# Optimization experiments

Hardware: AMD Instinct MI355X
Metric: run time of the kernel (lower is better)

The kernel has to match this reference:

```python
import jax, jax.numpy as jnp
import numpy as np

H = 16
QK_NOPE = 128
QK_ROPE = 64
QK_HEAD = 192
V_HEAD = 128
KV_LORA = 512
Q_LORA = 1536
HIDDEN = 2048
ROPE_THETA = 500000.0
EPS = 1e-6


def _rms_norm(x, w, eps=EPS):
    var = jnp.mean(x * x, axis=-1, keepdims=True)
    return w * (x * jax.lax.rsqrt(var + eps))


def _rotate_half(x):
    d = x.shape[-1] // 2
    return jnp.concatenate([-x[..., d:], x[..., :d]], axis=-1)


def _rope_cos_sin(T, dim, theta, dtype):
    inv_freq = 1.0 / (theta ** (jnp.arange(0, dim, 2, dtype=jnp.float32) / dim))
    t = jnp.arange(T, dtype=jnp.float32)
    freqs = jnp.outer(t, inv_freq)               # [T, dim//2]
    emb = jnp.concatenate([freqs, freqs], axis=-1)  # [T, dim]
    return jnp.cos(emb).astype(dtype), jnp.sin(emb).astype(dtype)


def _apply_rope_interleave(q, k, cos, sin):
    # deinterleave: [x0,x1,x2,...] -> [x0,x2,... , x1,x3,...]
    def deint(x):
        return jnp.concatenate([x[..., 0::2], x[..., 1::2]], axis=-1)
    q, k = deint(q), deint(k)
    cos = cos[None, None]  # [1,1,T,d]
    sin = sin[None, None]
    q_e = q * cos + _rotate_half(q) * sin
    k_e = k * cos + _rotate_half(k) * sin
    return q_e, k_e


def setup_inputs() -> dict:
    key = jax.random.key(0)
    ks = jax.random.split(key, 8)
    s = 0.02
    B, T = 2, 2048
    return {
        "x": jax.random.normal(ks[0], (B, T, HIDDEN), jnp.float32),
        "q_a_w": jax.random.normal(ks[1], (HIDDEN, Q_LORA), jnp.float32) * s,
        "q_a_ln_w": jnp.ones((Q_LORA,), jnp.float32),
        "q_b_w": jax.random.normal(ks[2], (Q_LORA, H * QK_HEAD), jnp.float32) * s,
        "kv_a_w": jax.random.normal(ks[3], (HIDDEN, KV_LORA + QK_ROPE), jnp.float32) * s,
        "kv_a_ln_w": jnp.ones((KV_LORA,), jnp.float32),
        "kv_b_w": jax.random.normal(ks[4], (KV_LORA, H * (QK_NOPE + V_HEAD)), jnp.float32) * s,
        "o_w": jax.random.normal(ks[5], (H * V_HEAD, HIDDEN), jnp.float32) * s,
    }


def reference(x, q_a_w, q_a_ln_w, q_b_w, kv_a_w, kv_a_ln_w, kv_b_w, o_w):
    B, T, _ = x.shape
    scale = QK_HEAD ** -0.5

    # Q path: hidden -> q_lora -> RMSNorm -> H*qk_head
    q = _rms_norm(x @ q_a_w, q_a_ln_w) @ q_b_w
    q = q.reshape(B, T, H, QK_HEAD).transpose(0, 2, 1, 3)  # [B,H,T,qk_head]
    q_nope, q_rope = q[..., :QK_NOPE], q[..., QK_NOPE:]

    # KV path: hidden -> kv_lora + rope_dim
    ckv = x @ kv_a_w
    kv_c, k_rope = ckv[..., :KV_LORA], ckv[..., KV_LORA:]
    kv = _rms_norm(kv_c, kv_a_ln_w) @ kv_b_w
    kv = kv.reshape(B, T, H, QK_NOPE + V_HEAD).transpose(0, 2, 1, 3)
    k_nope, v = kv[..., :QK_NOPE], kv[..., QK_NOPE:]

    k_rope = k_rope.reshape(B, 1, T, QK_ROPE)
    cos, sin = _rope_cos_sin(T, QK_ROPE, ROPE_THETA, x.dtype)
    q_rope, k_rope = _apply_rope_interleave(q_rope, k_rope, cos, sin)
    k_rope = jnp.broadcast_to(k_rope, (B, H, T, QK_ROPE))

    qf = jnp.concatenate([q_nope, q_rope], axis=-1)  # [B,H,T,192]
    kf = jnp.concatenate([k_nope, k_rope], axis=-1)

    # causal SDPA
    scores = jnp.einsum("bhqd,bhkd->bhqk", qf, kf) * scale
    causal = jnp.tril(jnp.ones((T, T), bool))
    scores = jnp.where(causal[None, None], scores, jnp.finfo(scores.dtype).min)
    attn = jax.nn.softmax(scores, axis=-1)
    out = jnp.einsum("bhqk,bhkd->bhqd", attn, v)  # [B,H,T,128]
    out = out.transpose(0, 2, 1, 3).reshape(B, T, H * V_HEAD)
    return out @ o_w
```

## Files before the change

kernel.cpp:

```cpp
#include <hip/hip_runtime.h>
#include <hip/hip_bf16.h>
#include <cstdint>


typedef __bf16 bf16;
typedef __bf16 bf16x8 __attribute__((ext_vector_type(8)));
typedef __bf16 bf16x4v __attribute__((ext_vector_type(4)));
typedef float f32x4 __attribute__((ext_vector_type(4)));

#define TSEQ 2048
#define MR 4096

typedef const uint32_t __attribute__((address_space(1))) * gas1_t;
typedef uint32_t __attribute__((address_space(3))) * las3_t;

static __device__ __forceinline__ void gload_lds16(const void* g, void* l) {
  __builtin_amdgcn_global_load_lds(
      reinterpret_cast<gas1_t>(reinterpret_cast<uintptr_t>(g)),
      reinterpret_cast<las3_t>(reinterpret_cast<uintptr_t>(l)), 16, 0, 0);
}

static __device__ __forceinline__ f32x4 mfma16(bf16x8 a, bf16x8 b, f32x4 c) {
  return __builtin_amdgcn_mfma_f32_16x16x32_bf16(a, b, c, 0, 0, 0);
}

static __device__ __forceinline__ void do_transpose(
    const float* __restrict__ W, bf16* __restrict__ Wt, int K, int N, int bi,
    int bj, float (*t)[33]) {
  int c = threadIdx.x & 31, r0 = threadIdx.x >> 5;
#pragma unroll
  for (int rr = 0; rr < 32; rr += 8)
    t[rr + r0][c] = W[(size_t)(bj * 32 + rr + r0) * N + bi * 32 + c];
  __syncthreads();
#pragma unroll
  for (int rr = 0; rr < 32; rr += 8)
    Wt[(size_t)(bi * 32 + rr + r0) * K + bj * 32 + c] = (bf16)t[c][rr + r0];
}

#define PREP_BLOCKS (8192 + 3072 + 1152 + 4608 + 2048 + 4096 + 192 + 256)

__global__ __launch_bounds__(256) void k_prep(
    const float* __restrict__ x, const float* __restrict__ q_a_w,
    const float* __restrict__ kv_a_w, const float* __restrict__ q_b_w,
    const float* __restrict__ kv_b_w, const float* __restrict__ o_w,
    bf16* __restrict__ x_bf, bf16* __restrict__ ab_wt,
    bf16* __restrict__ qb_wt, bf16* __restrict__ kvb_wt,
    bf16* __restrict__ o_wt, float* __restrict__ rt) {
  __shared__ float t[32][33];
  int nb = blockIdx.x;
  const int tid = threadIdx.x;
  if (nb < 8192) {
    int i = nb * 256 + tid;
    float4 f = reinterpret_cast<const float4*>(x)[i];
    bf16x4v o = {(bf16)f.x, (bf16)f.y, (bf16)f.z, (bf16)f.w};
    reinterpret_cast<bf16x4v*>(x_bf)[i] = o;
    return;
  }
  nb -= 8192;
  if (nb < 3072) { do_transpose(q_a_w, ab_wt, 2048, 1536, nb % 48, nb / 48, t); return; }
  nb -= 3072;
  if (nb < 1152) {
    do_transpose(kv_a_w, ab_wt + (size_t)1536 * 2048, 2048, 576, nb % 18, nb / 18, t);
    return;
  }
  nb -= 1152;
  if (nb < 4608) { do_transpose(q_b_w, qb_wt, 1536, 3072, nb % 96, nb / 96, t); return; }
  nb -= 4608;
  if (nb < 2048) { do_transpose(kv_b_w, kvb_wt, 512, 4096, nb % 128, nb / 128, t); return; }
  nb -= 2048;
  if (nb < 4096) { do_transpose(o_w, o_wt, 2048, 2048, nb % 64, nb / 64, t); return; }
  nb -= 4096;
  if (nb < 192) {
    uint4 z = make_uint4(0, 0, 0, 0);
    reinterpret_cast<uint4*>(ab_wt + (size_t)2112 * 2048)[nb * 256 + tid] = z;
    return;
  }
  nb -= 192;
  {
    int idx = nb * 256 + tid;
    int tt = idx >> 5, j = idx & 31;
    float freq = exp2f(-(float)j * (1.0f / 32.0f) * log2f(500000.0f));
    float ang = (float)tt * freq;
    rt[tt * 64 + 2 * j] = cosf(ang);
    rt[tt * 64 + 2 * j + 1] = sinf(ang);
  }
}

template <int NCH>
__global__ __launch_bounds__(64) void k_rmsnorm(const bf16* __restrict__ in,
                                                const float* __restrict__ w,
                                                bf16* __restrict__ out,
                                                int in_stride) {
  int row = blockIdx.x, lane = threadIdx.x;
  const int D = NCH * 512;
  const bf16* ip = in + (size_t)row * in_stride;
  bf16x8 v[NCH];
  float ss = 0.f;
#pragma unroll
  for (int c = 0; c < NCH; ++c) {
    v[c] = *reinterpret_cast<const bf16x8*>(ip + c * 512 + lane * 8);
#pragma unroll
    for (int e = 0; e < 8; ++e) { float f = (float)v[c][e]; ss += f * f; }
  }
#pragma unroll
  for (int m = 1; m <= 32; m <<= 1) ss += __shfl_xor(ss, m);
  float rs = rsqrtf(ss / (float)D + 1e-6f);
  bf16* op = out + (size_t)row * D;
#pragma unroll
  for (int c = 0; c < NCH; ++c) {
    bf16x8 o;
#pragma unroll
    for (int e = 0; e < 8; ++e)
      o[e] = (bf16)((float)v[c][e] * rs * w[c * 512 + lane * 8 + e]);
    *reinterpret_cast<bf16x8*>(op + c * 512 + lane * 8) = o;
  }
}

__global__ __launch_bounds__(64) void k_kv_norm_rope(
    const bf16* __restrict__ in, const float* __restrict__ w,
    const float* __restrict__ rt, bf16* __restrict__ kvn,
    bf16* __restrict__ kr, int in_stride) {
  int row = blockIdx.x, lane = threadIdx.x;
  const bf16* ip = in + (size_t)row * in_stride;
  bf16x8 v = *reinterpret_cast<const bf16x8*>(ip + lane * 8);
  float ss = 0.f;
#pragma unroll
  for (int e = 0; e < 8; ++e) { float f = (float)v[e]; ss += f * f; }
#pragma unroll
  for (int m = 1; m <= 32; m <<= 1) ss += __shfl_xor(ss, m);
  float rs = rsqrtf(ss / 512.0f + 1e-6f);
  bf16x8 o;
#pragma unroll
  for (int e = 0; e < 8; ++e) o[e] = (bf16)((float)v[e] * rs * w[lane * 8 + e]);
  *reinterpret_cast<bf16x8*>(kvn + (size_t)row * 512 + lane * 8) = o;
  if (lane < 32) {
    int t = row & (TSEQ - 1);
    float x0 = (float)ip[512 + 2 * lane], x1 = (float)ip[512 + 2 * lane + 1];
    float c = rt[t * 64 + 2 * lane], s = rt[t * 64 + 2 * lane + 1];
    kr[(size_t)row * 64 + lane] = (bf16)(x0 * c - x1 * s);
    kr[(size_t)row * 64 + 32 + lane] = (bf16)(x1 * c + x0 * s);
  }
}

__global__ __launch_bounds__(256) void k_rope_q(const bf16* __restrict__ q,
                                                const float* __restrict__ rt,
                                                bf16* __restrict__ qr) {
  int idx = blockIdx.x * 256 + threadIdx.x;
  int j = idx & 31, h = (idx >> 5) & 15, row = idx >> 9;
  int t = row & (TSEQ - 1);
  const bf16* src = q + (size_t)row * 3072 + h * 192 + 128;
  float x0 = (float)src[2 * j], x1 = (float)src[2 * j + 1];
  float c = rt[t * 64 + 2 * j], s = rt[t * 64 + 2 * j + 1];
  bf16* dst = qr + ((size_t)row * 16 + h) * 64;
  dst[j] = (bf16)(x0 * c - x1 * s);
  dst[32 + j] = (bf16)(x1 * c + x0 * s);
}

#define GPH(BUF, MH, KH, DO_READB, STAGE_STMT, WAIT_STMT)                     \
  {                                                                           \
    if (DO_READB) {                                                           \
      _Pragma("unroll") for (int ni = 0; ni < 4; ++ni) {                      \
        int row = wn * 64 + ni * 16 + lr;                                     \
        breg[KH][ni] = *reinterpret_cast<const bf16x8*>(                      \
            &Bs[BUF][row * 64 + ((((KH)*4 + lg) ^ (row & 7)) * 8)]);          \
      }                                                                       \
    }                                                                         \
    bf16x8 af[4];                                                             \
    _Pragma("unroll") for (int mi = 0; mi < 4; ++mi) {                        \
      int row = wm * 128 + (MH)*64 + mi * 16 + lr;                            \
      af[mi] = *reinterpret_cast<const bf16x8*>(                              \
          &As[BUF][row * 64 + ((((KH)*4 + lg) ^ (row & 7)) * 8)]);            \
    }                                                                         \
    STAGE_STMT;                                                               \
    __builtin_amdgcn_s_barrier();                                             \
    __builtin_amdgcn_s_setprio(1);                                            \
    _Pragma("unroll") for (int mi = 0; mi < 4; ++mi)                          \
        _Pragma("unroll") for (int ni = 0; ni < 4; ++ni)                      \
            acc[(MH)*4 + mi][ni] =                                            \
        mfma16(af[mi], breg[KH][ni], acc[(MH)*4 + mi][ni]);                   \
    __builtin_amdgcn_s_setprio(0);                                            \
    WAIT_STMT;                                                                \
    __builtin_amdgcn_s_barrier();                                             \
  }

template <bool OUT_F32>
__global__ __launch_bounds__(512, 2) void k_gemm8(const bf16* __restrict__ A,
                                                  const bf16* __restrict__ Bt,
                                                  void* __restrict__ C, int M,
                                                  int N, int K) {
  __shared__ bf16 As[2][256 * 64];
  __shared__ bf16 Bs[2][256 * 64];
  const int tid = threadIdx.x, lane = tid & 63, w = tid >> 6;
  const int lg = lane >> 4, lr = lane & 15;
  const int wm = w >> 2, wn = w & 3;
  const int nwg = gridDim.x * gridDim.y;
  const int orig = blockIdx.y * gridDim.x + blockIdx.x;
  const int cpx = nwg >> 3;
  const int wgid = (orig & 7) * cpx + (orig >> 3);
  const int m0 = (wgid / gridDim.x) * 256, n0 = (wgid % gridDim.x) * 256;
  const int T = K >> 7;

  f32x4 acc[8][4] = {};
  bf16x8 breg[2][4];

  auto stageA = [&](int tau, int h) {
    char* dst = (char*)&As[tau & 1][0] + h * 16384;
#pragma unroll
    for (int j = 0; j < 2; ++j) {
      int c = j * 512 + tid;
      int row = c >> 3, slot = c & 7;
      gload_lds16(A + (size_t)(m0 + h * 128 + row) * K + tau * 64 +
                      ((slot ^ (row & 7)) * 8),
                  dst + (size_t)(j * 512 + w * 64) * 16);
    }
  };
  auto stageB = [&](int tau, int h) {
    char* dst = (char*)&Bs[tau & 1][0] + h * 16384;
#pragma unroll
    for (int j = 0; j < 2; ++j) {
      int c = j * 512 + tid;
      int row = c >> 3, slot = c & 7;
      gload_lds16(Bt + (size_t)(n0 + h * 128 + row) * K + tau * 64 +
                      ((slot ^ (row & 7)) * 8),
                  dst + (size_t)(j * 512 + w * 64) * 16);
    }
  };

  stageB(0, 0); stageB(0, 1); stageA(0, 0); stageA(0, 1);
  stageB(1, 0); stageB(1, 1); stageA(1, 0);
  asm volatile("s_waitcnt vmcnt(6)" ::: "memory");
  __builtin_amdgcn_s_barrier();

  for (int t = 0; t < T - 1; ++t) {
    const int s2 = 2 * t + 2, s3 = 2 * t + 3, a1 = 2 * t + 1;
    GPH(0, 0, 0, true,  stageA(a1, 1), ((void)0));
    GPH(0, 0, 1, true,  stageB(s2, 0), ((void)0));
    GPH(0, 1, 0, false, stageB(s2, 1), ((void)0));
    GPH(0, 1, 1, false, stageA(s2, 0),
        asm volatile("s_waitcnt vmcnt(6)" ::: "memory"));
    GPH(1, 0, 0, true,  stageA(s2, 1), ((void)0));
    GPH(1, 0, 1, true,  stageB(s3, 0), ((void)0));
    GPH(1, 1, 0, false, stageB(s3, 1), ((void)0));
    GPH(1, 1, 1, false, stageA(s3, 0),
        asm volatile("s_waitcnt vmcnt(6)" ::: "memory"));
  }
  {
    const int a1 = 2 * T - 1;
    GPH(0, 0, 0, true,  stageA(a1, 1), ((void)0));
    GPH(0, 0, 1, true,  ((void)0),     ((void)0));
    GPH(0, 1, 0, false, ((void)0),     ((void)0));
    GPH(0, 1, 1, false, ((void)0),
        asm volatile("s_waitcnt vmcnt(0)" ::: "memory"));
    GPH(1, 0, 0, true,  ((void)0), ((void)0));
    GPH(1, 0, 1, true,  ((void)0), ((void)0));
    GPH(1, 1, 0, false, ((void)0), ((void)0));
    GPH(1, 1, 1, false, ((void)0), ((void)0));
  }

#pragma unroll
  for (int mi = 0; mi < 8; ++mi)
#pragma unroll
    for (int ni = 0; ni < 4; ++ni) {
      int col = n0 + wn * 64 + ni * 16 + lr;
#pragma unroll
      for (int r = 0; r < 4; ++r) {
        int rowg = m0 + wm * 128 + mi * 16 + lg * 4 + r;
        if (OUT_F32)
          reinterpret_cast<float*>(C)[(size_t)rowg * N + col] = acc[mi][ni][r];
        else
          reinterpret_cast<bf16*>(C)[(size_t)rowg * N + col] =
              (bf16)acc[mi][ni][r];
      }
    }
}

__global__ __launch_bounds__(512, 2) void k_attn(const bf16* __restrict__ q,
                                                 const bf16* __restrict__ qr,
                                                 const bf16* __restrict__ kv,
                                                 const bf16* __restrict__ kr,
                                                 bf16* __restrict__ o) {
  __shared__ bf16 Kn[2][64 * 128];
  __shared__ bf16 Kr[2][64 * 64];
  __shared__ bf16 Vs[2][64 * 128];
  __shared__ bf16 Ps[8 * 1024];
  const int tid = threadIdx.x, lane = tid & 63, w = tid >> 6;
  const int lg = lane >> 4, lr = lane & 15;
  const float qsc = 0.07216878364870323f * 1.44269504088896f;
  uint4 vreg[2];
  const int vrr = tid & 31, vvc = tid >> 5;

  for (int t = 0; t < 2; ++t) {
    const int id = t ? 511 - (int)blockIdx.x : (int)blockIdx.x;
    const int qt = 15 - (id >> 5);
    const int bh = id & 31;
    const int b = bh >> 4, h = bh & 15;
    const int q0 = qt * 128;
    const size_t rowbase = (size_t)b * TSEQ;
    const int nkt = 2 * qt + 2;
    const int qg = q0 + w * 16 + lr;

    auto issue_loads = [&](int kbase, int buf) {
#pragma unroll
      for (int kk = 0; kk < 2; ++kk)
        vreg[kk] = *reinterpret_cast<const uint4*>(
            kv + (rowbase + kbase + vrr * 2 + kk) * 4096 + h * 256 + 128 +
            vvc * 8);
#pragma unroll
      for (int i = 0; i < 2; ++i) {
        int c = i * 512 + tid;
        int row = c >> 4, j = c & 15;
        gload_lds16(
            kv + (rowbase + kbase + row) * 4096 + h * 256 +
                ((j ^ (row & 15)) * 8),
            (char*)&Kn[buf][0] + (size_t)(i * 512 + w * 64) * 16);
      }
      {
        int row = tid >> 3, j = tid & 7;
        gload_lds16(kr + (rowbase + kbase + row) * 64 + ((j ^ (row & 7)) * 8),
                    (char*)&Kr[buf][0] + (size_t)(w * 64) * 16);
      }
    };

    auto write_vs = [&](int buf) {
      const int kb0 = vrr * 2;
      const int cC = kb0 >> 5, g = (kb0 >> 3) & 3, j0 = kb0 & 7;
      const uint32_t* r0 = reinterpret_cast<const uint32_t*>(&vreg[0]);
      const uint32_t* r1 = reinterpret_cast<const uint32_t*>(&vreg[1]);
#pragma unroll
      for (int e = 0; e < 8; ++e) {
        uint32_t h0 = (r0[e >> 1] >> ((e & 1) * 16)) & 0xffffu;
        uint32_t h1 = (r1[e >> 1] >> ((e & 1) * 16)) & 0xffffu;
        int vd = vvc * 8 + e;
        int slot = (vd & 15) ^ g;
        *reinterpret_cast<uint32_t*>(
            &Vs[buf][((cC * 8 + (vd >> 4)) * 4 + g) * 128 + slot * 8 + j0]) =
            h0 | (h1 << 16);
      }
    };

    bf16x8 qf[6];
    {
      const bf16* qp = q + (rowbase + qg) * 3072 + h * 192;
#pragma unroll
      for (int dc = 0; dc < 4; ++dc) {
        bf16x8 v = *reinterpret_cast<const bf16x8*>(qp + dc * 32 + lg * 8);
#pragma unroll
        for (int e = 0; e < 8; ++e) v[e] = (bf16)((float)v[e] * qsc);
        qf[dc] = v;
      }
      const bf16* qrp = qr + ((rowbase + qg) * 16 + h) * 64;
#pragma unroll
      for (int dc = 0; dc < 2; ++dc) {
        bf16x8 v = *reinterpret_cast<const bf16x8*>(qrp + dc * 32 + lg * 8);
#pragma unroll
        for (int e = 0; e < 8; ++e) v[e] = (bf16)((float)v[e] * qsc);
        qf[4 + dc] = v;
      }
    }

    f32x4 oacc[8] = {};
    float m_run = -1e30f, l_run = 0.f;

    issue_loads(0, 0);
    write_vs(0);
    __syncthreads();

    for (int kt = 0; kt < nkt; ++kt) {
      const int kbase = kt * 64;
      const int buf = kt & 1;
      const bool more = (kt + 1 < nkt);
      if (more) issue_loads(kbase + 64, buf ^ 1);

      if (kbase <= q0 + w * 16 + 15) {
        f32x4 sacc[4];
#pragma unroll
        for (int kb = 0; kb < 4; ++kb) {
          const int row = kb * 16 + lr;
          bf16x8 kf[6];
#pragma unroll
          for (int dc = 0; dc < 4; ++dc)
            kf[dc] = *reinterpret_cast<const bf16x8*>(
                &Kn[buf][row * 128 + (((dc * 4 + lg) ^ (row & 15)) * 8)]);
#pragma unroll
          for (int dc = 0; dc < 2; ++dc)
            kf[4 + dc] = *reinterpret_cast<const bf16x8*>(
                &Kr[buf][row * 64 + (((dc * 4 + lg) ^ (row & 7)) * 8)]);
          __builtin_amdgcn_s_setprio(1);
          f32x4 sa = {0.f, 0.f, 0.f, 0.f};
#pragma unroll
          for (int dc = 0; dc < 6; ++dc) sa = mfma16(kf[dc], qf[dc], sa);
          sacc[kb] = sa;
          __builtin_amdgcn_s_setprio(0);
        }
        float sv[4][4];
        if (kbase + 63 <= q0 + w * 16) {
#pragma unroll
          for (int kb = 0; kb < 4; ++kb)
#pragma unroll
            for (int r = 0; r < 4; ++r) sv[kb][r] = sacc[kb][r];
        } else {
#pragma unroll
          for (int kb = 0; kb < 4; ++kb)
#pragma unroll
            for (int r = 0; r < 4; ++r) {
              int kgl = kbase + kb * 16 + lg * 4 + r;
              sv[kb][r] = (kgl <= qg) ? sacc[kb][r] : -1e30f;
            }
        }
        float pmax = -1e30f;
#pragma unroll
        for (int kb = 0; kb < 4; ++kb)
#pragma unroll
          for (int r = 0; r < 4; ++r) pmax = fmaxf(pmax, sv[kb][r]);
        pmax = fmaxf(pmax, __shfl_xor(pmax, 16));
        pmax = fmaxf(pmax, __shfl_xor(pmax, 32));
        if (!__all(pmax - m_run <= 8.0f)) {
          float mnew = fmaxf(m_run, pmax);
          float alpha = exp2f(m_run - mnew);
          l_run *= alpha;
#pragma unroll
          for (int vb = 0; vb < 8; ++vb) {
            oacc[vb][0] *= alpha; oacc[vb][1] *= alpha;
            oacc[vb][2] *= alpha; oacc[vb][3] *= alpha;
          }
          m_run = mnew;
        }
        float ls = 0.f;
#pragma unroll
        for (int kb = 0; kb < 4; ++kb) {
          bf16x4v pw;
#pragma unroll
          for (int r = 0; r < 4; ++r) {
            float p = exp2f(sv[kb][r] - m_run);
            ls += p;
            pw[r] = (bf16)p;
          }
          *reinterpret_cast<bf16x4v*>(
              &Ps[w * 1024 + lr * 64 +
                  (((kb * 2 + (lg >> 1)) ^ (lr & 7)) * 8) + (lg & 1) * 4]) = pw;
        }
        ls += __shfl_xor(ls, 16);
        ls += __shfl_xor(ls, 32);
        l_run += ls;
#pragma unroll
        for (int c = 0; c < 2; ++c) {
          bf16x8 pb = *reinterpret_cast<const bf16x8*>(
              &Ps[w * 1024 + lr * 64 + (((c * 4 + lg) ^ (lr & 7)) * 8)]);
          __builtin_amdgcn_s_setprio(1);
#pragma unroll
          for (int vb = 0; vb < 8; ++vb) {
            bf16x8 av = *reinterpret_cast<const bf16x8*>(
                &Vs[buf][((c * 8 + vb) * 4 + lg) * 128 + (lr ^ lg) * 8]);
            oacc[vb] = mfma16(av, pb, oacc[vb]);
          }
          __builtin_amdgcn_s_setprio(0);
        }
      }
      if (more) write_vs(buf ^ 1);
      __syncthreads();
    }

    bf16* Os = &Kn[0][0] + w * 2048;
    {
      float inv = 1.0f / l_run;
#pragma unroll
      for (int vb = 0; vb < 8; ++vb) {
        bf16x4v ov;
#pragma unroll
        for (int r = 0; r < 4; ++r) ov[r] = (bf16)(oacc[vb][r] * inv);
        int slot16 = vb * 2 + (lg >> 1);
        *reinterpret_cast<bf16x4v*>(
            &Os[lr * 128 + ((slot16 ^ (lr & 7)) * 8) + (lg & 1) * 4]) = ov;
      }
    }
    asm volatile("s_waitcnt lgkmcnt(0)");
    __builtin_amdgcn_sched_barrier(0);
#pragma unroll
    for (int i = 0; i < 4; ++i) {
      const int r = i * 4 + lg;
      bf16x8 ov = *reinterpret_cast<const bf16x8*>(
          &Os[r * 128 + ((lr ^ (r & 7)) * 8)]);
      *reinterpret_cast<bf16x8*>(
          o + (rowbase + q0 + w * 16 + r) * 2048 + h * 128 + lr * 8) = ov;
    }
    __syncthreads();
  }
}

extern "C" void kernel_launch(void* const* d_in, const int* in_sizes, int n_in,
                              void* d_out, int out_size, void* d_ws,
                              size_t ws_size, hipStream_t stream) {
  (void)in_sizes; (void)n_in; (void)out_size; (void)ws_size;
  const float* x       = (const float*)d_in[0];
  const float* q_a_w   = (const float*)d_in[1];
  const float* q_a_ln  = (const float*)d_in[2];
  const float* q_b_w   = (const float*)d_in[3];
  const float* kv_a_w  = (const float*)d_in[4];
  const float* kv_a_ln = (const float*)d_in[5];
  const float* kv_b_w  = (const float*)d_in[6];
  const float* o_w     = (const float*)d_in[7];

  char* ws = (char*)d_ws;
  size_t off = 0;
  auto alloc = [&](size_t bytes) {
    void* p = ws + off;
    off += (bytes + 255) & ~(size_t)255;
    return p;
  };
  bf16* x_bf   = (bf16*)alloc((size_t)MR * 2048 * 2);
  bf16* ab_wt  = (bf16*)alloc((size_t)2304 * 2048 * 2);
  bf16* qb_wt  = (bf16*)alloc((size_t)3072 * 1536 * 2);
  bf16* kvb_wt = (bf16*)alloc((size_t)4096 * 512 * 2);
  bf16* o_wt   = (bf16*)alloc((size_t)2048 * 2048 * 2);
  float* rt    = (float*)alloc((size_t)2048 * 64 * 4);
  bf16* qac    = (bf16*)alloc((size_t)MR * 2304 * 2);
  bf16* q_a_n  = (bf16*)alloc((size_t)MR * 1536 * 2);
  bf16* kv_c_n = (bf16*)alloc((size_t)MR * 512 * 2);
  bf16* kr     = (bf16*)alloc((size_t)MR * 64 * 2);
  bf16* qbuf   = (bf16*)alloc((size_t)MR * 3072 * 2);
  bf16* qr     = (bf16*)alloc((size_t)MR * 16 * 64 * 2);
  bf16* kvbuf  = (bf16*)alloc((size_t)MR * 4096 * 2);
  bf16* attn_o = (bf16*)alloc((size_t)MR * 2048 * 2);

  k_prep<<<PREP_BLOCKS, 256, 0, stream>>>(x, q_a_w, kv_a_w, q_b_w, kv_b_w,
                                          o_w, x_bf, ab_wt, qb_wt, kvb_wt,
                                          o_wt, rt);
  k_gemm8<false><<<dim3(9, 16), 512, 0, stream>>>(x_bf, ab_wt, qac, MR, 2304, 2048);
  k_rmsnorm<3><<<MR, 64, 0, stream>>>(qac, q_a_ln, q_a_n, 2304);
  k_kv_norm_rope<<<MR, 64, 0, stream>>>(qac + 1536, kv_a_ln, rt, kv_c_n, kr, 2304);
  k_gemm8<false><<<dim3(12, 16), 512, 0, stream>>>(q_a_n, qb_wt, qbuf, MR, 3072, 1536);
  k_rope_q<<<8192, 256, 0, stream>>>(qbuf, rt, qr);
  k_gemm8<false><<<dim3(16, 16), 512, 0, stream>>>(kv_c_n, kvb_wt, kvbuf, MR, 4096, 512);
  k_attn<<<dim3(256), 512, 0, stream>>>(qbuf, qr, kvbuf, kr, attn_o);
  k_gemm8<true><<<dim3(8, 16), 512, 0, stream>>>(attn_o, o_wt, d_out, MR, 2048, 2048);
}
```

Before: 287.2 us.

## Merge the two norm kernels and run q_b/kv_b GEMMs in one launch

```diff
diff --git a/kernel.cpp b/kernel.cpp
--- a/kernel.cpp
+++ b/kernel.cpp
@@ -86,56 +86,48 @@
   }
 }
 
-template <int NCH>
-__global__ __launch_bounds__(64) void k_rmsnorm(const bf16* __restrict__ in,
-                                                const float* __restrict__ w,
-                                                bf16* __restrict__ out,
-                                                int in_stride) {
+__global__ __launch_bounds__(64) void k_norms(
+    const bf16* __restrict__ qac, const float* __restrict__ qw,
+    const float* __restrict__ kvw, const float* __restrict__ rt,
+    bf16* __restrict__ q_a_n, bf16* __restrict__ kv_c_n,
+    bf16* __restrict__ kr) {
   int row = blockIdx.x, lane = threadIdx.x;
-  const int D = NCH * 512;
-  const bf16* ip = in + (size_t)row * in_stride;
-  bf16x8 v[NCH];
+  const bf16* ip = qac + (size_t)row * 2304;
+  bf16x8 v[3];
   float ss = 0.f;
 #pragma unroll
-  for (int c = 0; c < NCH; ++c) {
+  for (int c = 0; c < 3; ++c) {
     v[c] = *reinterpret_cast<const bf16x8*>(ip + c * 512 + lane * 8);
 #pragma unroll
     for (int e = 0; e < 8; ++e) { float f = (float)v[c][e]; ss += f * f; }
   }
 #pragma unroll
   for (int m = 1; m <= 32; m <<= 1) ss += __shfl_xor(ss, m);
-  float rs = rsqrtf(ss / (float)D + 1e-6f);
-  bf16* op = out + (size_t)row * D;
-#pragma unroll
-  for (int c = 0; c < NCH; ++c) {
+  float rs = rsqrtf(ss / 1536.0f + 1e-6f);
+  bf16* op = q_a_n + (size_t)row * 1536;
+#pragma unroll
+  for (int c = 0; c < 3; ++c) {
     bf16x8 o;
 #pragma unroll
     for (int e = 0; e < 8; ++e)
-      o[e] = (bf16)((float)v[c][e] * rs * w[c * 512 + lane * 8 + e]);
+      o[e] = (bf16)((float)v[c][e] * rs * qw[c * 512 + lane * 8 + e]);
     *reinterpret_cast<bf16x8*>(op + c * 512 + lane * 8) = o;
   }
-}
-
-__global__ __launch_bounds__(64) void k_kv_norm_rope(
-    const bf16* __restrict__ in, const float* __restrict__ w,
-    const float* __restrict__ rt, bf16* __restrict__ kvn,
-    bf16* __restrict__ kr, int in_stride) {
-  int row = blockIdx.x, lane = threadIdx.x;
-  const bf16* ip = in + (size_t)row * in_stride;
-  bf16x8 v = *reinterpret_cast<const bf16x8*>(ip + lane * 8);
-  float ss = 0.f;
-#pragma unroll
-  for (int e = 0; e < 8; ++e) { float f = (float)v[e]; ss += f * f; }
-#pragma unroll
-  for (int m = 1; m <= 32; m <<= 1) ss += __shfl_xor(ss, m);
-  float rs = rsqrtf(ss / 512.0f + 1e-6f);
-  bf16x8 o;
-#pragma unroll
-  for (int e = 0; e < 8; ++e) o[e] = (bf16)((float)v[e] * rs * w[lane * 8 + e]);
-  *reinterpret_cast<bf16x8*>(kvn + (size_t)row * 512 + lane * 8) = o;
+  bf16x8 kvv = *reinterpret_cast<const bf16x8*>(ip + 1536 + lane * 8);
+  float s2 = 0.f;
+#pragma unroll
+  for (int e = 0; e < 8; ++e) { float f = (float)kvv[e]; s2 += f * f; }
+#pragma unroll
+  for (int m = 1; m <= 32; m <<= 1) s2 += __shfl_xor(s2, m);
+  float rs2 = rsqrtf(s2 / 512.0f + 1e-6f);
+  bf16x8 o2;
+#pragma unroll
+  for (int e = 0; e < 8; ++e)
+    o2[e] = (bf16)((float)kvv[e] * rs2 * kvw[lane * 8 + e]);
+  *reinterpret_cast<bf16x8*>(kv_c_n + (size_t)row * 512 + lane * 8) = o2;
   if (lane < 32) {
     int t = row & (TSEQ - 1);
-    float x0 = (float)ip[512 + 2 * lane], x1 = (float)ip[512 + 2 * lane + 1];
+    float x0 = (float)ip[2048 + 2 * lane], x1 = (float)ip[2048 + 2 * lane + 1];
     float c = rt[t * 64 + 2 * lane], s = rt[t * 64 + 2 * lane + 1];
     kr[(size_t)row * 64 + lane] = (bf16)(x0 * c - x1 * s);
     kr[(size_t)row * 64 + 32 + lane] = (bf16)(x1 * c + x0 * s);
@@ -184,20 +176,14 @@
   }
 
 template <bool OUT_F32>
-__global__ __launch_bounds__(512, 2) void k_gemm8(const bf16* __restrict__ A,
-                                                  const bf16* __restrict__ Bt,
-                                                  void* __restrict__ C, int M,
-                                                  int N, int K) {
-  __shared__ bf16 As[2][256 * 64];
-  __shared__ bf16 Bs[2][256 * 64];
+static __device__ __forceinline__ void gemm8_body(
+    const bf16* __restrict__ A, const bf16* __restrict__ Bt,
+    void* __restrict__ C, int N, int K, int bi, int bj, bf16 (*As)[16384],
+    bf16 (*Bs)[16384]) {
   const int tid = threadIdx.x, lane = tid & 63, w = tid >> 6;
   const int lg = lane >> 4, lr = lane & 15;
   const int wm = w >> 2, wn = w & 3;
-  const int nwg = gridDim.x * gridDim.y;
-  const int orig = blockIdx.y * gridDim.x + blockIdx.x;
-  const int cpx = nwg >> 3;
-  const int wgid = (orig & 7) * cpx + (orig >> 3);
-  const int m0 = (wgid / gridDim.x) * 256, n0 = (wgid % gridDim.x) * 256;
+  const int m0 = bj * 256, n0 = bi * 256;
   const int T = K >> 7;
 
   f32x4 acc[8][4] = {};
@@ -272,6 +258,37 @@
               (bf16)acc[mi][ni][r];
       }
     }
+}
+
+template <bool OUT_F32>
+__global__ __launch_bounds__(512, 2) void k_gemm8(const bf16* __restrict__ A,
+                                                  const bf16* __restrict__ Bt,
+                                                  void* __restrict__ C, int N,
+                                                  int K) {
+  __shared__ bf16 As[2][16384];
+  __shared__ bf16 Bs[2][16384];
+  const int nwg = gridDim.x * gridDim.y;
+  const int orig = blockIdx.y * gridDim.x + blockIdx.x;
+  const int wgid = (orig & 7) * (nwg >> 3) + (orig >> 3);
+  gemm8_body<OUT_F32>(A, Bt, C, N, K, wgid % gridDim.x, wgid / gridDim.x, As,
+                      Bs);
+}
+
+__global__ __launch_bounds__(512, 2) void k_gemm8_dual(
+    const bf16* __restrict__ A1, const bf16* __restrict__ B1,
+    bf16* __restrict__ C1, const bf16* __restrict__ A2,
+    const bf16* __restrict__ B2, bf16* __restrict__ C2) {
+  __shared__ bf16 As[2][16384];
+  __shared__ bf16 Bs[2][16384];
+  int id = blockIdx.x;
+  if (id < 192) {
+    int wg = (id & 7) * 24 + (id >> 3);
+    gemm8_body<false>(A1, B1, C1, 3072, 1536, wg % 12, wg / 12, As, Bs);
+  } else {
+    int s = id - 192;
+    int wg = (s & 7) * 32 + (s >> 3);
+    gemm8_body<false>(A2, B2, C2, 4096, 512, wg % 16, wg / 16, As, Bs);
+  }
 }
 
 __global__ __launch_bounds__(512, 2) void k_attn(const bf16* __restrict__ q,
@@ -525,12 +542,11 @@
   k_prep<<<PREP_BLOCKS, 256, 0, stream>>>(x, q_a_w, kv_a_w, q_b_w, kv_b_w,
                                           o_w, x_bf, ab_wt, qb_wt, kvb_wt,
                                           o_wt, rt);
-  k_gemm8<false><<<dim3(9, 16), 512, 0, stream>>>(x_bf, ab_wt, qac, MR, 2304, 2048);
-  k_rmsnorm<3><<<MR, 64, 0, stream>>>(qac, q_a_ln, q_a_n, 2304);
-  k_kv_norm_rope<<<MR, 64, 0, stream>>>(qac + 1536, kv_a_ln, rt, kv_c_n, kr, 2304);
-  k_gemm8<false><<<dim3(12, 16), 512, 0, stream>>>(q_a_n, qb_wt, qbuf, MR, 3072, 1536);
+  k_gemm8<false><<<dim3(9, 16), 512, 0, stream>>>(x_bf, ab_wt, qac, 2304, 2048);
+  k_norms<<<MR, 64, 0, stream>>>(qac, q_a_ln, kv_a_ln, rt, q_a_n, kv_c_n, kr);
+  k_gemm8_dual<<<dim3(448), 512, 0, stream>>>(q_a_n, qb_wt, qbuf, kv_c_n,
+                                              kvb_wt, kvbuf);
   k_rope_q<<<8192, 256, 0, stream>>>(qbuf, rt, qr);
-  k_gemm8<false><<<dim3(16, 16), 512, 0, stream>>>(kv_c_n, kvb_wt, kvbuf, MR, 4096, 512);
   k_attn<<<dim3(256), 512, 0, stream>>>(qbuf, qr, kvbuf, kr, attn_o);
-  k_gemm8<true><<<dim3(8, 16), 512, 0, stream>>>(attn_o, o_wt, d_out, MR, 2048, 2048);
-}
+  k_gemm8<true><<<dim3(8, 16), 512, 0, stream>>>(attn_o, o_wt, d_out, 2048, 2048);
+}
```

After: 278.4 us (median of 2 runs). 3.1% less time.
